# Optimization experiments

Hardware: AMD Instinct MI355X
Metric: run time of the kernel (lower is better)

## Reference

```python
import jax, jax.numpy as jnp
import numpy as np

HEADS = 8
DIM_HEAD = 32
SCALE = DIM_HEAD ** -0.5
EPS = 1e-5


def _layernorm_gamma(x, gamma):
    # GammaLayerNorm: zero-mean/unit-var over last dim, learnable gamma, no bias
    mu = jnp.mean(x, axis=-1, keepdims=True)
    var = jnp.var(x, axis=-1, keepdims=True)
    return (x - mu) * jax.lax.rsqrt(var + EPS) * gamma


def setup_inputs() -> dict:
    key = jax.random.key(0)
    k1, k2, k3 = jax.random.split(key, 3)
    B, N, D = 8, 16384, 256
    hidden = HEADS * DIM_HEAD  # 256
    x = jax.random.normal(k1, (B, N, D), dtype=jnp.float32)
    Wqkv = jax.random.normal(k2, (D, 3 * hidden), dtype=jnp.float32) * (D ** -0.5)
    Wout = jax.random.normal(k3, (hidden, D), dtype=jnp.float32) * (hidden ** -0.5)
    gamma = jnp.ones((D,), dtype=jnp.float32)
    return {"x": x, "Wqkv": Wqkv, "Wout": Wout, "gamma": gamma}


def reference(x, Wqkv, Wout, gamma):
    B, N, D = x.shape
    qkv = x @ Wqkv  # [B, N, 3*hidden]
    q, k, v = jnp.split(qkv, 3, axis=-1)

    def to_heads(t):  # b n (h d) -> b h n d
        return t.reshape(B, N, HEADS, DIM_HEAD).transpose(0, 2, 1, 3)

    q, k, v = map(to_heads, (q, k, v))
    q = jax.nn.softmax(q, axis=-1) * SCALE  # softmax over feature dim d
    k = jax.nn.softmax(k, axis=2)           # softmax over token dim n
    context = jnp.einsum('bhnd,bhne->bhde', k, v)  # [B,H,d,e] small kv state
    out = jnp.einsum('bhde,bhnd->bhne', context, q)  # [B,H,N,e]
    out = out.transpose(0, 2, 1, 3).reshape(B, N, HEADS * DIM_HEAD)
    out = out @ Wout
    return _layernorm_gamma(out, gamma)
```

## Files before the change

### kernel.cpp

```cpp
#include <hip/hip_runtime.h>
#include <hip/hip_bf16.h>

typedef __attribute__((ext_vector_type(8))) short short8;
typedef __attribute__((ext_vector_type(4))) float f32x4;

constexpr int SEQ = 16384, BATCH = 8, DIN = 256, NQKV = 768;
constexpr float SCALE = 0.17677669529663687f;
constexpr float EPS = 1e-5f;

__device__ __forceinline__ unsigned short f2bf(float f){
  __hip_bfloat16 h = __float2bfloat16(f);
  unsigned short u; __builtin_memcpy(&u, &h, 2); return u;
}
__device__ __forceinline__ float bf2f(unsigned short h){
  return __uint_as_float(((unsigned int)h) << 16);
}
__device__ __forceinline__ void gload_lds16(const void* g, void* l){
  __builtin_amdgcn_global_load_lds(
    (const __attribute__((address_space(1))) unsigned int*)g,
    (__attribute__((address_space(3))) unsigned int*)l, 16, 0, 0);
}
__device__ __forceinline__ void lds_barrier(){
  asm volatile("s_waitcnt lgkmcnt(0)" ::: "memory");
  __builtin_amdgcn_s_barrier();
}

__global__ void k_wt(const float* __restrict__ W, unsigned short* __restrict__ WT){
  int id = blockIdx.x * 256 + threadIdx.x;
  int k = id / NQKV, n = id % NQKV;
  WT[n * DIN + k] = f2bf(W[id]);
}

__global__ __launch_bounds__(512) void k_qkv(const float* __restrict__ X,
                                             const unsigned short* __restrict__ WT,
                                             unsigned short* __restrict__ Q,
                                             float* __restrict__ ctxg,
                                             float* __restrict__ sumg){
  __shared__ unsigned short Bs[2][32 * 256];
  __shared__ unsigned short WVs[2][32][264];
  __shared__ float sumLds[256];
  const int blk = blockIdx.x;
  const size_t m0 = (size_t)blk * 256;
  const int b = blk >> 6;
  const int tid = threadIdx.x, wave = tid >> 6, lane = tid & 63;
  const int lg = lane >> 4, li = lane & 15;
  if (tid < 256) sumLds[tid] = 0.f;
  unsigned short* qs = &WVs[0][0][0];

  auto panelN0 = [](int p){
    return (p < 16) ? (((p & 1) ? 512 : 256) + (p >> 1) * 32) : (p - 16) * 32;
  };
  auto stageB = [&](int buf, int n0){
    #pragma unroll
    for (int it = 0; it < 2; it++){
      int L = (it * 512 + tid) * 16;
      int G = L ^ (((L >> 9) & 7) << 4);
      gload_lds16((const char*)WT + (size_t)(n0 + (L >> 9)) * 512 + (G & 511),
                  (char*)Bs[buf] + L);
    }
  };

  stageB(0, panelN0(0));
  short8 afrag[2][8];
  #pragma unroll
  for (int rt = 0; rt < 2; rt++){
    const float* xr = X + (m0 + wave * 32 + rt * 16 + li) * 256 + lg * 8;
    #pragma unroll
    for (int ks = 0; ks < 8; ks++){
      float4 f0 = *reinterpret_cast<const float4*>(xr + ks * 32);
      float4 f1 = *reinterpret_cast<const float4*>(xr + ks * 32 + 4);
      short8 a;
      a[0] = f2bf(f0.x); a[1] = f2bf(f0.y); a[2] = f2bf(f0.z); a[3] = f2bf(f0.w);
      a[4] = f2bf(f1.x); a[5] = f2bf(f1.y); a[6] = f2bf(f1.z); a[7] = f2bf(f1.w);
      afrag[rt][ks] = a;
    }
  }
  #pragma unroll
  for (int rt = 0; rt < 2; rt++)
    #pragma unroll
    for (int ks = 0; ks < 8; ks++)
      asm volatile("" : "+v"(afrag[rt][ks]));
  __syncthreads();

  const f32x4 zf = {0.f, 0.f, 0.f, 0.f};
  int buf = 0;
  #pragma unroll 1
  for (int p = 0; p < 24; ++p){
    if (p < 23) stageB(buf ^ 1, panelN0(p + 1));
    f32x4 acc[2][2];
    acc[0][0] = zf; acc[0][1] = zf; acc[1][0] = zf; acc[1][1] = zf;
    __builtin_amdgcn_s_setprio(1);
    #pragma unroll
    for (int ks = 0; ks < 8; ks++)
      #pragma unroll
      for (int j = 0; j < 2; j++){
        int nl = j * 16 + li;
        int L = nl * 512 + (ks * 32 + lg * 8) * 2;
        short8 bb = *reinterpret_cast<const short8*>((const char*)Bs[buf] + (L ^ ((nl & 7) << 4)));
        acc[0][j] = __builtin_amdgcn_mfma_f32_16x16x32_bf16(afrag[0][ks], bb, acc[0][j], 0, 0, 0);
        acc[1][j] = __builtin_amdgcn_mfma_f32_16x16x32_bf16(afrag[1][ks], bb, acc[1][j], 0, 0, 0);
      }
    __builtin_amdgcn_s_setprio(0);
    if (p < 16){
      int h = p >> 1;
      if (!(p & 1)){
        #pragma unroll
        for (int j = 0; j < 2; j++){
          float cs = 0.f;
          #pragma unroll
          for (int rt = 0; rt < 2; rt++){
            unsigned short h0 = f2bf(__expf(acc[rt][j][0]));
            unsigned short h1 = f2bf(__expf(acc[rt][j][1]));
            unsigned short h2 = f2bf(__expf(acc[rt][j][2]));
            unsigned short h3 = f2bf(__expf(acc[rt][j][3]));
            cs += bf2f(h0) + bf2f(h1) + bf2f(h2) + bf2f(h3);
            ushort4 pk; pk.x = h0; pk.y = h1; pk.z = h2; pk.w = h3;
            *reinterpret_cast<ushort4*>(&WVs[0][j * 16 + li][wave * 32 + rt * 16 + lg * 4]) = pk;
          }
          cs += __shfl_xor(cs, 16); cs += __shfl_xor(cs, 32);
          if (lane < 16) atomicAdd(&sumLds[h * 32 + j * 16 + li], cs);
        }
      } else {
        #pragma unroll
        for (int j = 0; j < 2; j++)
          #pragma unroll
          for (int rt = 0; rt < 2; rt++){
            ushort4 pk;
            pk.x = f2bf(acc[rt][j][0]); pk.y = f2bf(acc[rt][j][1]);
            pk.z = f2bf(acc[rt][j][2]); pk.w = f2bf(acc[rt][j][3]);
            *reinterpret_cast<ushort4*>(&WVs[1][j * 16 + li][wave * 32 + rt * 16 + lg * 4]) = pk;
          }
      }
      __syncthreads();
      if (p & 1){
        int th = wave >> 2, dh = (wave >> 1) & 1, eh = wave & 1;
        f32x4 c = zf;
        #pragma unroll
        for (int ks = 0; ks < 4; ks++){
          short8 aw = *reinterpret_cast<const short8*>(&WVs[0][dh * 16 + li][th * 128 + ks * 32 + lg * 8]);
          short8 bv = *reinterpret_cast<const short8*>(&WVs[1][eh * 16 + li][th * 128 + ks * 32 + lg * 8]);
          c = __builtin_amdgcn_mfma_f32_16x16x32_bf16(aw, bv, c, 0, 0, 0);
        }
        float* cp = ctxg + ((size_t)(b * 8 + h)) * 1024;
        #pragma unroll
        for (int r = 0; r < 4; r++)
          atomicAdd(&cp[(dh * 16 + lg * 4 + r) * 32 + eh * 16 + li], c[r]);
        lds_barrier();
      }
    } else {
      int ph = p - 16;
      #pragma unroll
      for (int rt = 0; rt < 2; rt++)
        #pragma unroll
        for (int j = 0; j < 2; j++)
          #pragma unroll
          for (int r = 0; r < 4; r++)
            qs[(wave * 32 + rt * 16 + lg * 4 + r) * 40 + j * 16 + li]
              = f2bf(acc[rt][j][r]);
      lds_barrier();
      {
        int row = tid >> 2, c8 = (tid & 3) * 8;
        #pragma unroll
        for (int rr = 0; rr < 2; rr++){
          short8 v = *reinterpret_cast<const short8*>(&qs[(rr * 128 + row) * 40 + c8]);
          *reinterpret_cast<short8*>(&Q[(m0 + rr * 128 + row) * 256 + ph * 32 + c8]) = v;
        }
      }
      __syncthreads();
    }
    buf ^= 1;
  }
  if (tid < 256) atomicAdd(&sumg[b * 256 + tid], sumLds[tid]);
}

__global__ __launch_bounds__(256) void k_build_m(const float* __restrict__ ctxg,
                                                 const float* __restrict__ sumg,
                                                 const float* __restrict__ Wout,
                                                 unsigned short* __restrict__ MT){
  __shared__ float ctxs[32][33];
  __shared__ float swb[32];
  int b = blockIdx.x >> 3, h = blockIdx.x & 7;
  int t = threadIdx.x;
  int e = t & 31, dq = t >> 5;
  const float* cg = ctxg + (size_t)blockIdx.x * 1024;
  if (t < 32) swb[t] = sumg[b * 256 + h * 32 + t];
  __syncthreads();
  ctxs[dq][e]      = cg[dq * 32 + e]        / swb[dq];
  ctxs[dq + 8][e]  = cg[(dq + 8) * 32 + e]  / swb[dq + 8];
  ctxs[dq + 16][e] = cg[(dq + 16) * 32 + e] / swb[dq + 16];
  ctxs[dq + 24][e] = cg[(dq + 24) * 32 + e] / swb[dq + 24];
  __syncthreads();
  float s[32];
  #pragma unroll
  for (int d = 0; d < 32; d++) s[d] = 0.f;
  for (int ee = 0; ee < 32; ee++){
    float wv = Wout[(size_t)(h * 32 + ee) * 256 + t];
    #pragma unroll
    for (int d = 0; d < 32; d++) s[d] += ctxs[d][ee] * wv;
  }
  unsigned short* mp = MT + (size_t)b * 65536 + (size_t)t * 256 + h * 32;
  #pragma unroll
  for (int d8 = 0; d8 < 4; d8++){
    short8 pk;
    #pragma unroll
    for (int q = 0; q < 8; q++) pk[q] = (short)f2bf(s[d8 * 8 + q]);
    *reinterpret_cast<short8*>(mp + d8 * 8) = pk;
  }
}

__global__ __launch_bounds__(256, 4) void k_out(const unsigned short* __restrict__ Qm,
                                                const unsigned short* __restrict__ MT,
                                                const float* __restrict__ gamma,
                                                float* __restrict__ out){
  __shared__ unsigned short Bs[64 * 256];
  const int blk = blockIdx.x;
  const int b = blk >> 8;
  const size_t m0 = (size_t)blk * 64;
  const int tid = threadIdx.x, wave = tid >> 6, lane = tid & 63;
  const int lg = lane >> 4, li = lane & 15;

  short8 afrag[8];
  {
    const unsigned short* qr = Qm + (m0 + wave * 16 + li) * 256 + lg * 8;
    #pragma unroll
    for (int ks = 0; ks < 8; ks++)
      afrag[ks] = *reinterpret_cast<const short8*>(qr + ks * 32);
  }
  #pragma unroll
  for (int ks = 0; ks < 8; ks++){
    float v[8];
    #pragma unroll
    for (int q = 0; q < 8; q++) v[q] = bf2f((unsigned short)afrag[ks][q]);
    float mx = v[0];
    #pragma unroll
    for (int q = 1; q < 8; q++) mx = fmaxf(mx, v[q]);
    mx = fmaxf(mx, __shfl_xor(mx, 16));
    mx = fmaxf(mx, __shfl_xor(mx, 32));
    float s = 0.f;
    #pragma unroll
    for (int q = 0; q < 8; q++){ v[q] = __expf(v[q] - mx); s += v[q]; }
    s += __shfl_xor(s, 16);
    s += __shfl_xor(s, 32);
    float iv = SCALE / s;
    #pragma unroll
    for (int q = 0; q < 8; q++) afrag[ks][q] = (short)f2bf(v[q] * iv);
  }

  const char* mtb = (const char*)MT + (size_t)b * 131072;
  f32x4 acc[4][4];
  const f32x4 zf = {0.f, 0.f, 0.f, 0.f};
  #pragma unroll
  for (int jb = 0; jb < 4; jb++)
    #pragma unroll
    for (int j = 0; j < 4; j++) acc[jb][j] = zf;

  #pragma unroll
  for (int jb = 0; jb < 4; jb++){
    if (jb) __syncthreads();
    #pragma unroll
    for (int rr = 0; rr < 8; rr++){
      int L = rr * 4096 + tid * 16;
      int G = L ^ (((L >> 9) & 7) << 4);
      gload_lds16(mtb + (size_t)jb * 32768 + G, (char*)Bs + L);
    }
    __syncthreads();
    #pragma unroll
    for (int ks = 0; ks < 8; ks++)
      #pragma unroll
      for (int j = 0; j < 4; j++){
        int n = j * 16 + li;
        int L = n * 512 + (ks * 32 + lg * 8) * 2;
        short8 bb = *reinterpret_cast<const short8*>((const char*)Bs + (L ^ ((n & 7) << 4)));
        acc[jb][j] = __builtin_amdgcn_mfma_f32_16x16x32_bf16(afrag[ks], bb, acc[jb][j], 0, 0, 0);
      }
  }

  float gam[16];
  #pragma unroll
  for (int jb = 0; jb < 4; jb++)
    #pragma unroll
    for (int j = 0; j < 4; j++) gam[jb * 4 + j] = gamma[jb * 64 + j * 16 + li];
  #pragma unroll
  for (int r = 0; r < 4; r++){
    float s = 0.f, qq = 0.f;
    #pragma unroll
    for (int jb = 0; jb < 4; jb++)
      #pragma unroll
      for (int j = 0; j < 4; j++){ float v = acc[jb][j][r]; s += v; qq += v * v; }
    #pragma unroll
    for (int mm = 1; mm < 16; mm <<= 1){ s += __shfl_xor(s, mm); qq += __shfl_xor(qq, mm); }
    float mu = s * (1.f / 256.f);
    float var = qq * (1.f / 256.f) - mu * mu;
    float inv = rsqrtf(var + EPS);
    float* op = out + (m0 + wave * 16 + lg * 4 + r) * 256;
    #pragma unroll
    for (int jb = 0; jb < 4; jb++)
      #pragma unroll
      for (int j = 0; j < 4; j++)
        op[jb * 64 + j * 16 + li] = (acc[jb][j][r] - mu) * inv * gam[jb * 4 + j];
  }
}

extern "C" void kernel_launch(void* const* d_in, const int* in_sizes, int n_in,
                              void* d_out, int out_size, void* d_ws, size_t ws_size,
                              hipStream_t stream){
  const float* x     = (const float*)d_in[0];
  const float* Wqkv  = (const float*)d_in[1];
  const float* Wout  = (const float*)d_in[2];
  const float* gamma = (const float*)d_in[3];
  float* out = (float*)d_out;

  char* ws = (char*)d_ws;
  size_t off = 0;
  unsigned short* Q   = (unsigned short*)(ws + off); off += (size_t)BATCH * SEQ * 256 * 2;
  unsigned short* WT  = (unsigned short*)(ws + off); off += (size_t)NQKV * DIN * 2;
  float* ctxg         = (float*)(ws + off);          off += (size_t)64 * 1024 * 4;
  float* sumg         = (float*)(ws + off);          off += (size_t)BATCH * 256 * 4;
  unsigned short* MT  = (unsigned short*)(ws + off); off += (size_t)BATCH * 65536 * 2;

  k_wt<<<(NQKV * DIN) / 256, 256, 0, stream>>>(Wqkv, WT);
  hipMemsetAsync(ctxg, 0, (size_t)64 * 1024 * 4 + (size_t)BATCH * 256 * 4, stream);
  k_qkv<<<512, 512, 0, stream>>>(x, WT, Q, ctxg, sumg);
  k_build_m<<<64, 256, 0, stream>>>(ctxg, sumg, Wout, MT);
  k_out<<<2048, 256, 0, stream>>>(Q, MT, gamma, out);
}
```

Measured before the change: 212.4 us.

## Halve qkv block to 128 rows and single-buffer weight panels

The fused QKV projection kernel now uses 256-thread blocks over 128 rows each, launched as 1024 blocks instead of 512. The weight-panel LDS staging drops from double to single buffering: the next panel load is issued after the barrier and overlaps the context MFMA or Q store epilogue. This cuts LDS per block, allowing more resident blocks and shorter tail imbalance. In exchange, the prefetch overlaps only the epilogue rather than the main MFMA loop, and the context atomics per head double because there are twice as many blocks.

```diff
diff --git a/kernel.cpp b/kernel.cpp
--- a/kernel.cpp
+++ b/kernel.cpp
@@ -31,36 +31,36 @@
   WT[n * DIN + k] = f2bf(W[id]);
 }
 
-__global__ __launch_bounds__(512) void k_qkv(const float* __restrict__ X,
+__global__ __launch_bounds__(256) void k_qkv(const float* __restrict__ X,
                                              const unsigned short* __restrict__ WT,
                                              unsigned short* __restrict__ Q,
                                              float* __restrict__ ctxg,
                                              float* __restrict__ sumg){
-  __shared__ unsigned short Bs[2][32 * 256];
-  __shared__ unsigned short WVs[2][32][264];
+  __shared__ unsigned short Bs[32 * 256];
+  __shared__ unsigned short WVs[2][32][136];
   __shared__ float sumLds[256];
   const int blk = blockIdx.x;
-  const size_t m0 = (size_t)blk * 256;
-  const int b = blk >> 6;
+  const size_t m0 = (size_t)blk * 128;
+  const int b = blk >> 7;
   const int tid = threadIdx.x, wave = tid >> 6, lane = tid & 63;
   const int lg = lane >> 4, li = lane & 15;
-  if (tid < 256) sumLds[tid] = 0.f;
+  sumLds[tid] = 0.f;
   unsigned short* qs = &WVs[0][0][0];
 
   auto panelN0 = [](int p){
     return (p < 16) ? (((p & 1) ? 512 : 256) + (p >> 1) * 32) : (p - 16) * 32;
   };
-  auto stageB = [&](int buf, int n0){
-    #pragma unroll
-    for (int it = 0; it < 2; it++){
-      int L = (it * 512 + tid) * 16;
+  auto stageB = [&](int n0){
+    #pragma unroll
+    for (int it = 0; it < 4; it++){
+      int L = (it * 256 + tid) * 16;
       int G = L ^ (((L >> 9) & 7) << 4);
       gload_lds16((const char*)WT + (size_t)(n0 + (L >> 9)) * 512 + (G & 511),
-                  (char*)Bs[buf] + L);
+                  (char*)Bs + L);
     }
   };
 
-  stageB(0, panelN0(0));
+  stageB(panelN0(0));
   short8 afrag[2][8];
   #pragma unroll
   for (int rt = 0; rt < 2; rt++){
@@ -83,10 +83,8 @@
   __syncthreads();
 
   const f32x4 zf = {0.f, 0.f, 0.f, 0.f};
-  int buf = 0;
   #pragma unroll 1
   for (int p = 0; p < 24; ++p){
-    if (p < 23) stageB(buf ^ 1, panelN0(p + 1));
     f32x4 acc[2][2];
     acc[0][0] = zf; acc[0][1] = zf; acc[1][0] = zf; acc[1][1] = zf;
     __builtin_amdgcn_s_setprio(1);
@@ -96,7 +94,7 @@
       for (int j = 0; j < 2; j++){
         int nl = j * 16 + li;
         int L = nl * 512 + (ks * 32 + lg * 8) * 2;
-        short8 bb = *reinterpret_cast<const short8*>((const char*)Bs[buf] + (L ^ ((nl & 7) << 4)));
+        short8 bb = *reinterpret_cast<const short8*>((const char*)Bs + (L ^ ((nl & 7) << 4)));
         acc[0][j] = __builtin_amdgcn_mfma_f32_16x16x32_bf16(afrag[0][ks], bb, acc[0][j], 0, 0, 0);
         acc[1][j] = __builtin_amdgcn_mfma_f32_16x16x32_bf16(afrag[1][ks], bb, acc[1][j], 0, 0, 0);
       }
@@ -131,24 +129,7 @@
             *reinterpret_cast<ushort4*>(&WVs[1][j * 16 + li][wave * 32 + rt * 16 + lg * 4]) = pk;
           }
       }
-      __syncthreads();
-      if (p & 1){
-        int th = wave >> 2, dh = (wave >> 1) & 1, eh = wave & 1;
-        f32x4 c = zf;
-        #pragma unroll
-        for (int ks = 0; ks < 4; ks++){
-          short8 aw = *reinterpret_cast<const short8*>(&WVs[0][dh * 16 + li][th * 128 + ks * 32 + lg * 8]);
-          short8 bv = *reinterpret_cast<const short8*>(&WVs[1][eh * 16 + li][th * 128 + ks * 32 + lg * 8]);
-          c = __builtin_amdgcn_mfma_f32_16x16x32_bf16(aw, bv, c, 0, 0, 0);
-        }
-        float* cp = ctxg + ((size_t)(b * 8 + h)) * 1024;
-        #pragma unroll
-        for (int r = 0; r < 4; r++)
-          atomicAdd(&cp[(dh * 16 + lg * 4 + r) * 32 + eh * 16 + li], c[r]);
-        lds_barrier();
-      }
     } else {
-      int ph = p - 16;
       #pragma unroll
       for (int rt = 0; rt < 2; rt++)
         #pragma unroll
@@ -157,20 +138,35 @@
           for (int r = 0; r < 4; r++)
             qs[(wave * 32 + rt * 16 + lg * 4 + r) * 40 + j * 16 + li]
               = f2bf(acc[rt][j][r]);
-      lds_barrier();
-      {
-        int row = tid >> 2, c8 = (tid & 3) * 8;
-        #pragma unroll
-        for (int rr = 0; rr < 2; rr++){
-          short8 v = *reinterpret_cast<const short8*>(&qs[(rr * 128 + row) * 40 + c8]);
-          *reinterpret_cast<short8*>(&Q[(m0 + rr * 128 + row) * 256 + ph * 32 + c8]) = v;
-        }
-      }
-      __syncthreads();
-    }
-    buf ^= 1;
-  }
-  if (tid < 256) atomicAdd(&sumg[b * 256 + tid], sumLds[tid]);
+    }
+    __syncthreads();
+    if (p < 23) stageB(panelN0(p + 1));
+    if (p < 16 && (p & 1)){
+      int h = p >> 1;
+      int dh = wave >> 1, eh = wave & 1;
+      f32x4 c = zf;
+      #pragma unroll
+      for (int ks = 0; ks < 4; ks++){
+        short8 aw = *reinterpret_cast<const short8*>(&WVs[0][dh * 16 + li][ks * 32 + lg * 8]);
+        short8 bv = *reinterpret_cast<const short8*>(&WVs[1][eh * 16 + li][ks * 32 + lg * 8]);
+        c = __builtin_amdgcn_mfma_f32_16x16x32_bf16(aw, bv, c, 0, 0, 0);
+      }
+      float* cp = ctxg + ((size_t)(b * 8 + h)) * 1024;
+      #pragma unroll
+      for (int r = 0; r < 4; r++)
+        atomicAdd(&cp[(dh * 16 + lg * 4 + r) * 32 + eh * 16 + li], c[r]);
+    } else if (p >= 16){
+      int ph = p - 16;
+      int row = tid >> 2, c8 = (tid & 3) * 8;
+      #pragma unroll
+      for (int rr = 0; rr < 2; rr++){
+        short8 v = *reinterpret_cast<const short8*>(&qs[(rr * 64 + row) * 40 + c8]);
+        *reinterpret_cast<short8*>(&Q[(m0 + rr * 64 + row) * 256 + ph * 32 + c8]) = v;
+      }
+    }
+    if (p < 23) __syncthreads();
+  }
+  atomicAdd(&sumg[b * 256 + tid], sumLds[tid]);
 }
 
 __global__ __launch_bounds__(256) void k_build_m(const float* __restrict__ ctxg,
@@ -320,7 +316,7 @@
 
   k_wt<<<(NQKV * DIN) / 256, 256, 0, stream>>>(Wqkv, WT);
   hipMemsetAsync(ctxg, 0, (size_t)64 * 1024 * 4 + (size_t)BATCH * 256 * 4, stream);
-  k_qkv<<<512, 512, 0, stream>>>(x, WT, Q, ctxg, sumg);
+  k_qkv<<<1024, 256, 0, stream>>>(x, WT, Q, ctxg, sumg);
   k_build_m<<<64, 256, 0, stream>>>(ctxg, sumg, Wout, MT);
   k_out<<<2048, 256, 0, stream>>>(Q, MT, gamma, out);
 }
```

Result: faster. 192.3 us (-9.5%).
